# Kernel optimization log

Measured on AMD Instinct MI355X. Metric: run time of the kernel, lower is better.

Reference implementation:

```python
import jax, jax.numpy as jnp
import numpy as np

B, T, Rn, D, O, E, H, C, TM = 20, 20, 20, 4096, 16, 512, 8, 68, 1900


def l2norm(x, axis=-1, eps=1e-12):
    return x / jnp.maximum(jnp.linalg.norm(x, axis=axis, keepdims=True), eps)


def setup_inputs() -> dict:
    key = jax.random.key(0)
    ks = jax.random.split(key, 10)
    return {
        "features": jax.random.normal(ks[0], (B, T, Rn, D), jnp.float32),
        "labels": jax.random.randint(ks[1], (B, O), 0, C),
        "temporal_mem": jax.random.normal(ks[2], (TM, T, D), jnp.float32),
        "entity_W": jax.random.normal(ks[3], (C, E), jnp.float32) / np.float32(np.sqrt(C)),
        "entity_b": jnp.zeros((E,), jnp.float32),
        "Wq": jax.random.normal(ks[4], (E, E), jnp.float32) / np.float32(np.sqrt(E)),
        "Wk": jax.random.normal(ks[5], (D, E), jnp.float32) / np.float32(np.sqrt(D)),
        "Wv": jax.random.normal(ks[6], (D, E), jnp.float32) / np.float32(np.sqrt(D)),
        "Wo": jax.random.normal(ks[7], (E, E), jnp.float32) / np.float32(np.sqrt(E)),
        "obj_W1": jax.random.normal(ks[8], (D, E), jnp.float32) / np.float32(np.sqrt(D)),
        "obj_b1": jnp.zeros((E,), jnp.float32),
        "obj_W2": jax.random.normal(ks[9], (E, 1), jnp.float32) / np.float32(np.sqrt(E)),
        "obj_b2": jnp.zeros((1,), jnp.float32),
    }


def reference(features, labels, temporal_mem, entity_W, entity_b, Wq, Wk, Wv, Wo,
              obj_W1, obj_b1, obj_W2, obj_b2):
    beta = 0.5   # loss mixing weight (module's beta)
    qgce = 0.7   # generalized-CE exponent
    Dh = E // H
    # region features, L2-normalized (dataset_feat == 'CVPR' path)
    Rf = l2norm(features)                                   # [B,T,Rn,D]

    # ---- temporal memory-bank kNN retrieval ----
    R_max = l2norm(jnp.max(Rf, axis=2))                     # [B,T,D] max-pool over regions
    mem_max = l2norm(jnp.max(temporal_mem, axis=1))         # [TM,D] max-pool over frames
    sim = jnp.einsum('btd,md->btm', R_max, mem_max)         # [B,T,TM]
    idx = jnp.argmax(sim, axis=-1)                          # [B,T] nearest memory slot
    Rp = temporal_mem[idx]                                  # [B,T,T,D] gathered memory videos
    mem_feat = jnp.max(Rp, axis=2)                          # [B,T,D]

    # ---- entity (object-label) embedding: one-hot with class 0 zeroed ----
    onehot = jax.nn.one_hot(labels, C, dtype=features.dtype)
    onehot = onehot * (labels != 0)[..., None].astype(features.dtype)
    Qe = onehot @ entity_W + entity_b                       # [B,O,E]

    # ---- multi-head attention fusion over regions + retrieved memory ----
    kv = jnp.concatenate([Rf.reshape(B, T * Rn, D), mem_feat], axis=1)  # [B,N,D]
    q = (Qe @ Wq).reshape(B, O, H, Dh)
    k = (kv @ Wk).reshape(B, -1, H, Dh)
    v = (kv @ Wv).reshape(B, -1, H, Dh)
    scores = jnp.einsum('bohd,bnhd->bhon', q, k) / np.float32(np.sqrt(Dh))
    attn = jax.nn.softmax(scores, axis=-1)
    fused = jnp.einsum('bhon,bnhd->bohd', attn, v).reshape(B, O, E) @ Wo  # [B,O,E]

    # ---- top-k region objectness selection + generalized CE ----
    QR = jax.lax.stop_gradient(jnp.mean(scores, axis=1)[:, :, :T * Rn].reshape(B, O, T, Rn))
    hi = jnp.argmax(QR, axis=-1)                            # [B,O,T] top-1 region
    lo = jnp.argmin(QR, axis=-1)                            # [B,O,T] low region
    bidx = jnp.arange(B)[:, None, None]
    tidx = jnp.arange(T)[None, None, :]
    R_high = Rf[bidx, tidx, hi]                             # [B,O,T,D]
    R_low = Rf[bidx, tidx, lo]                              # [B,O,T,D]
    osel = (labels != 0).astype(features.dtype)             # [B,O]
    onum = jnp.maximum(jnp.sum(osel, axis=1), 1.0)
    mlp = lambda x: jax.nn.sigmoid(jnp.tanh(x @ obj_W1 + obj_b1) @ obj_W2 + obj_b2)
    s_hi = mlp(R_high * osel[..., None, None]).squeeze(-1)  # [B,O,T]
    s_lo = mlp(R_low * osel[..., None, None]).squeeze(-1)
    gce_hi = jnp.mean((1.0 - (s_hi + 1e-7) ** qgce) / qgce * osel[..., None], axis=-1)
    gce_lo = jnp.mean((1.0 - (1.0 - s_lo + 1e-7) ** qgce) / qgce * osel[..., None], axis=-1)
    gce = jnp.mean(jnp.sum(gce_hi, axis=1) / onum) + jnp.mean(jnp.sum(gce_lo, axis=1) / onum)

    return fused + beta * gce
```

## Files before the change

### kernel.cpp

```cpp
#include <hip/hip_runtime.h>

#define B_   20
#define T_   20
#define RN   20
#define D_   4096
#define O_   16
#define E_   512
#define H_   8
#define DH   64
#define TM_  1900
#define NKV  420
#define MROWS (B_*NKV)
#define MPAD 8448
#define NW   1536
#define NSIM 1920
#define MSIM 512
#define CAP  256
#define SIMK 4

using f32x4  = __attribute__((ext_vector_type(4))) float;
using bf16x8 = __attribute__((ext_vector_type(8))) __bf16;

__device__ __forceinline__ unsigned short f2bf(float f){
  unsigned u = __float_as_uint(f);
  u += 0x7fffu + ((u >> 16) & 1u);
  return (unsigned short)(u >> 16);
}

__device__ __forceinline__ void st_bf4(unsigned short* dst, float4 v){
  ushort4 o = make_ushort4(f2bf(v.x), f2bf(v.y), f2bf(v.z), f2bf(v.w));
  *(ushort4*)dst = o;
}

__device__ __forceinline__ float bsum256(float v, float* sh){
  int t = threadIdx.x;
  for (int o = 32; o; o >>= 1) v += __shfl_down(v, o, 64);
  __syncthreads();
  if ((t & 63) == 0) sh[t >> 6] = v;
  __syncthreads();
  return sh[0] + sh[1] + sh[2] + sh[3];
}

__device__ __forceinline__ float bmax256(float v, float* sh){
  int t = threadIdx.x;
  for (int o = 32; o; o >>= 1) v = fmaxf(v, __shfl_down(v, o, 64));
  __syncthreads();
  if ((t & 63) == 0) sh[t >> 6] = v;
  __syncthreads();
  return fmaxf(fmaxf(sh[0], sh[1]), fmaxf(sh[2], sh[3]));
}

__device__ __forceinline__ void gld16(const void* g, void* l){
  __builtin_amdgcn_global_load_lds(
      (const __attribute__((address_space(1))) unsigned int*)g,
      (__attribute__((address_space(3))) unsigned int*)l, 16, 0, 0);
}

__global__ __launch_bounds__(256) void k_wt(const float* __restrict__ Wk, const float* __restrict__ Wv,
                                            const float* __restrict__ W1, unsigned short* __restrict__ Wall){
  __shared__ float tile[32][33];
  int kb = blockIdx.x * 32, nb = blockIdx.y * 32;
  const float* src; int nc0;
  if (nb < 512)      { src = Wk; nc0 = nb; }
  else if (nb < 1024){ src = Wv; nc0 = nb - 512; }
  else               { src = W1; nc0 = nb - 1024; }
  int tx = threadIdx.x, ty = threadIdx.y;
  for (int j = 0; j < 4; ++j){
    int k = kb + ty + j*8;
    tile[ty + j*8][tx] = src[(size_t)k*E_ + nc0 + tx];
  }
  __syncthreads();
  for (int j = 0; j < 4; ++j){
    int n = nb + ty + j*8;
    int k = kb + tx;
    Wall[(size_t)n*D_ + k] = f2bf(tile[tx][ty + j*8]);
  }
}

__global__ __launch_bounds__(256) void k_region(const float* __restrict__ F, unsigned short* __restrict__ A,
                                                float* __restrict__ rmaxr, float* __restrict__ rmsum,
                                                unsigned short* __restrict__ ubf){
  int bt = blockIdx.x, t = threadIdx.x;
  if (bt >= 400){
    int4 z = make_int4(0,0,0,0);
    int4* row = (int4*)(ubf + (size_t)bt*D_);
    row[t] = z; row[t + 256] = z;
    return;
  }
  int b = bt / T_, tt = bt % T_;
  const float* fb = F + (size_t)bt*RN*D_;
  unsigned short* ab = A + ((size_t)b*NKV + (size_t)tt*RN)*D_;
  __shared__ float sh[4];
  float4 mx[4];
#pragma unroll
  for (int i = 0; i < 4; ++i) mx[i] = make_float4(-1e30f,-1e30f,-1e30f,-1e30f);
  for (int r = 0; r < RN; ++r){
    float4 v[4];
    float s = 0.f;
#pragma unroll
    for (int i = 0; i < 4; ++i){
      v[i] = *(const float4*)(fb + (size_t)r*D_ + i*1024 + t*4);
      s += v[i].x*v[i].x + v[i].y*v[i].y + v[i].z*v[i].z + v[i].w*v[i].w;
    }
    s = bsum256(s, sh);
    float ri = 1.f / fmaxf(sqrtf(s), 1e-12f);
#pragma unroll
    for (int i = 0; i < 4; ++i){
      v[i].x *= ri; v[i].y *= ri; v[i].z *= ri; v[i].w *= ri;
      st_bf4(ab + (size_t)r*D_ + i*1024 + t*4, v[i]);
      mx[i].x = fmaxf(mx[i].x, v[i].x); mx[i].y = fmaxf(mx[i].y, v[i].y);
      mx[i].z = fmaxf(mx[i].z, v[i].z); mx[i].w = fmaxf(mx[i].w, v[i].w);
    }
  }
  float s2 = 0.f;
#pragma unroll
  for (int i = 0; i < 4; ++i){
    *(float4*)(rmaxr + (size_t)bt*D_ + i*1024 + t*4) = mx[i];
    s2 += mx[i].x*mx[i].x + mx[i].y*mx[i].y + mx[i].z*mx[i].z + mx[i].w*mx[i].w;
  }
  s2 = bsum256(s2, sh);
  if (t == 0) rmsum[bt] = s2;
  float inv = 1.f / fmaxf(sqrtf(s2), 1e-12f);
#pragma unroll
  for (int i = 0; i < 4; ++i){
    float4 u = mx[i];
    u.x *= inv; u.y *= inv; u.z *= inv; u.w *= inv;
    st_bf4(ubf + (size_t)bt*D_ + i*1024 + t*4, u);
  }
}

__global__ __launch_bounds__(256) void k_mempool(const float* __restrict__ TMm, float* __restrict__ umax,
                                                 float* __restrict__ msum, unsigned short* __restrict__ wnorm){
  int m = blockIdx.x, t = threadIdx.x;
  if (m >= TM_){
    int4 z = make_int4(0,0,0,0);
    int4* row = (int4*)(wnorm + (size_t)m*D_);
    row[t] = z; row[t + 256] = z;
    return;
  }
  const float* base = TMm + (size_t)m*T_*D_;
  float4 mx[4];
#pragma unroll
  for (int i = 0; i < 4; ++i) mx[i] = make_float4(-1e30f,-1e30f,-1e30f,-1e30f);
  for (int f = 0; f < T_; ++f){
#pragma unroll
    for (int i = 0; i < 4; ++i){
      float4 v = *(const float4*)(base + (size_t)f*D_ + i*1024 + t*4);
      mx[i].x = fmaxf(mx[i].x, v.x); mx[i].y = fmaxf(mx[i].y, v.y);
      mx[i].z = fmaxf(mx[i].z, v.z); mx[i].w = fmaxf(mx[i].w, v.w);
    }
  }
  float s = 0.f;
#pragma unroll
  for (int i = 0; i < 4; ++i){
    *(float4*)(umax + (size_t)m*D_ + i*1024 + t*4) = mx[i];
    s += mx[i].x*mx[i].x + mx[i].y*mx[i].y + mx[i].z*mx[i].z + mx[i].w*mx[i].w;
  }
  __shared__ float sh[4];
  s = bsum256(s, sh);
  if (t == 0) msum[m] = s;
  float inv = 1.f / fmaxf(sqrtf(s), 1e-12f);
#pragma unroll
  for (int i = 0; i < 4; ++i){
    float4 u = mx[i];
    u.x *= inv; u.y *= inv; u.z *= inv; u.w *= inv;
    st_bf4(wnorm + (size_t)m*D_ + i*1024 + t*4, u);
  }
}

__global__ __launch_bounds__(256, 2) void k_gemm(const unsigned short* __restrict__ A,
                                                 const unsigned short* __restrict__ Bw,
                                                 float* __restrict__ C,
                                                 int nNt, int ldc, int doswz, int nwg,
                                                 int nblk, int nkt, size_t cpart){
  __shared__ char lds[32768];
  int part = blockIdx.x / nblk;
  int bid  = blockIdx.x % nblk;
  if (doswz){ int q = nwg >> 3; bid = (bid & 7)*q + (bid >> 3); }
  int mt = bid / nNt, nt = bid % nNt;
  int tid = threadIdx.x, wv = tid >> 6, l = tid & 63;
  int wr = (wv >> 1) * 64, wc = (wv & 1) * 64;
  const char* Ab = (const char*)A + (size_t)mt*128*(size_t)(D_*2);
  const char* Bb = (const char*)Bw + (size_t)nt*128*(size_t)(D_*2);
  C += (size_t)part * cpart;
  f32x4 acc[4][4];
#pragma unroll
  for (int m = 0; m < 4; ++m)
#pragma unroll
    for (int n = 0; n < 4; ++n) acc[m][n] = (f32x4){0.f,0.f,0.f,0.f};
  int kt0 = part * nkt;
  for (int kt = kt0; kt < kt0 + nkt; ++kt){
    int ktoff = kt*128;
#pragma unroll
    for (int i = 0; i < 4; ++i){
      int idx = i*256 + tid;
      int row = idx >> 3, u = idx & 7;
      int ul = u ^ (row & 7);
      gld16(Ab + (size_t)row*(D_*2) + ktoff + ul*16, lds + i*4096 + wv*1024);
      gld16(Bb + (size_t)row*(D_*2) + ktoff + ul*16, lds + 16384 + i*4096 + wv*1024);
    }
    __syncthreads();
#pragma unroll
    for (int kk = 0; kk < 2; ++kk){
      bf16x8 av[4], bv[4];
#pragma unroll
      for (int m = 0; m < 4; ++m){
        int row = wr + m*16 + (l & 15);
        int u = (kk*4 + (l >> 4)) ^ (row & 7);
        av[m] = *(const bf16x8*)(lds + row*128 + u*16);
      }
#pragma unroll
      for (int n = 0; n < 4; ++n){
        int row = wc + n*16 + (l & 15);
        int u = (kk*4 + (l >> 4)) ^ (row & 7);
        bv[n] = *(const bf16x8*)(lds + 16384 + row*128 + u*16);
      }
#pragma unroll
      for (int m = 0; m < 4; ++m)
#pragma unroll
        for (int n = 0; n < 4; ++n)
          acc[m][n] = __builtin_amdgcn_mfma_f32_16x16x32_bf16(av[m], bv[n], acc[m][n], 0, 0, 0);
    }
    __syncthreads();
  }
  int rq = (l >> 4) * 4, cq = l & 15;
  size_t crow0 = (size_t)mt*128 + wr, ccol0 = (size_t)nt*128 + wc;
#pragma unroll
  for (int m = 0; m < 4; ++m)
#pragma unroll
    for (int n = 0; n < 4; ++n){
      size_t r0 = crow0 + m*16 + rq, c0 = ccol0 + n*16 + cq;
#pragma unroll
      for (int j = 0; j < 4; ++j)
        C[(r0 + j)*ldc + c0] = acc[m][n][j];
    }
}

__global__ __launch_bounds__(256) void k_pick(const float* __restrict__ simp,
                                              const float* __restrict__ rmaxr, const float* __restrict__ rmsum,
                                              const float* __restrict__ umax, const float* __restrict__ msum,
                                              unsigned short* __restrict__ A){
  int bt = blockIdx.x, t = threadIdx.x;
  if (bt >= 400){
    int4 z = make_int4(0,0,0,0);
    int4* row = (int4*)(A + (size_t)(MROWS + bt - 400)*D_);
    row[t] = z; row[t + 256] = z;
    return;
  }
  __shared__ float srow[NSIM];
  __shared__ float sh[4];
  __shared__ int cnt;
  __shared__ int cl[CAP];
  for (int m = t; m < NSIM; m += 256){
    float s = 0.f;
#pragma unroll
    for (int p = 0; p < SIMK; ++p)
      s += simp[(size_t)p*MSIM*NSIM + (size_t)bt*NSIM + m];
    srow[m] = s;
  }
  if (t == 0) cnt = 0;
  __syncthreads();
  float mx = -1e30f;
  for (int m = t; m < TM_; m += 256) mx = fmaxf(mx, srow[m]);
  mx = bmax256(mx, sh);
  float thr = mx - 2.5e-4f;
  for (int m = t; m < TM_; m += 256){
    if (srow[m] >= thr){
      int p = atomicAdd(&cnt, 1);
      if (p < CAP) cl[p] = m;
    }
  }
  __syncthreads();
  int cn = cnt < CAP ? cnt : CAP;
  float rinvv = 1.f / fmaxf(sqrtf(rmsum[bt]), 1e-12f);
  const float* a = rmaxr + (size_t)bt*D_;
  float best = -1e30f; int bestm = 0;
  for (int ci = 0; ci < cn; ++ci){
    int m = cl[ci];
    const float* wrow = umax + (size_t)m*D_;
    float p = 0.f;
    for (int i = t*4; i < D_; i += 1024){
      float4 av = *(const float4*)(a + i);
      float4 wv = *(const float4*)(wrow + i);
      p += av.x*wv.x + av.y*wv.y + av.z*wv.z + av.w*wv.w;
    }
    p = bsum256(p, sh);
    float sim = p * rinvv * (1.f / fmaxf(sqrtf(msum[m]), 1e-12f));
    if (sim > best || (sim == best && m < bestm) || ci == 0){ 
      if (sim > best || ci == 0 || (sim == best && m < bestm)){ best = sim; bestm = m; }
    }
  }
  int b = bt / T_, tt = bt % T_;
  unsigned short* dst = A + ((size_t)b*NKV + 400 + tt)*D_;
  const float* src = umax + (size_t)bestm*D_;
#pragma unroll
  for (int i = 0; i < 4; ++i){
    size_t off = (size_t)i*1024 + t*4;
    float4 v = *(const float4*)(src + off);
    st_bf4(dst + off, v);
  }
}

__global__ __launch_bounds__(256) void k_q(const int* __restrict__ labels, const float* __restrict__ entW,
                                           const float* __restrict__ entB, const float* __restrict__ Wq,
                                           float* __restrict__ q){
  int bo = blockIdx.x, t = threadIdx.x;
  __shared__ float qe[E_];
  int lab = labels[bo];
  float sel = (lab != 0) ? 1.f : 0.f;
  qe[t]       = sel * entW[(size_t)lab*E_ + t]       + entB[t];
  qe[t + 256] = sel * entW[(size_t)lab*E_ + t + 256] + entB[t + 256];
  __syncthreads();
  float a0 = 0.f, a1 = 0.f;
  for (int ep = 0; ep < E_; ++ep){
    float r = qe[ep];
    a0 += r * Wq[(size_t)ep*E_ + t];
    a1 += r * Wq[(size_t)ep*E_ + t + 256];
  }
  q[(size_t)bo*E_ + t] = a0;
  q[(size_t)bo*E_ + t + 256] = a1;
}

__global__ __launch_bounds__(256) void k_attn(const float* __restrict__ q, const float* __restrict__ c2,
                                              float* __restrict__ fpre){
  int bh = blockIdx.x; int b = bh >> 3, h = bh & 7;
  int t = threadIdx.x, w = t >> 6, l = t & 63;
  __shared__ float qhp[O_][DH + 1];
  __shared__ float kb[105][DH + 1];
  __shared__ float sc[O_][NKV];
  for (int i = t; i < O_*DH; i += 256){
    int o = i >> 6, d = i & 63;
    qhp[o][d] = q[((size_t)(b*O_ + o))*E_ + h*DH + d] * 0.125f;
  }
  __syncthreads();
  for (int c = 0; c < 4; ++c){
    for (int i = t; i < 105*DH; i += 256){
      int j = i >> 6, d = i & 63;
      kb[j][d] = c2[((size_t)(b*NKV + c*105 + j))*NW + h*DH + d];
    }
    __syncthreads();
    for (int i = t; i < O_*105; i += 256){
      int o = i / 105, j = i % 105;
      float acc = 0.f;
      for (int d = 0; d < DH; ++d) acc += qhp[o][d] * kb[j][d];
      sc[o][c*105 + j] = acc;
    }
    __syncthreads();
  }
  for (int oi = 0; oi < 4; ++oi){
    int o = w + oi*4;
    float mx = -1e30f;
    for (int n = l; n < NKV; n += 64) mx = fmaxf(mx, sc[o][n]);
    for (int off = 32; off; off >>= 1) mx = fmaxf(mx, __shfl_xor(mx, off, 64));
    float sum = 0.f;
    for (int n = l; n < NKV; n += 64){ float e = expf(sc[o][n] - mx); sc[o][n] = e; sum += e; }
    for (int off = 32; off; off >>= 1) sum += __shfl_xor(sum, off, 64);
    float inv = 1.f / sum;
    for (int n = l; n < NKV; n += 64) sc[o][n] *= inv;
  }
  __syncthreads();
  float acc[4] = {0.f, 0.f, 0.f, 0.f};
  for (int c = 0; c < 4; ++c){
    for (int i = t; i < 105*DH; i += 256){
      int j = i >> 6, d = i & 63;
      kb[j][d] = c2[((size_t)(b*NKV + c*105 + j))*NW + E_ + h*DH + d];
    }
    __syncthreads();
#pragma unroll
    for (int og = 0; og < 4; ++og){
      int o = og*4 + w;
      float a = 0.f;
      for (int j = 0; j < 105; ++j) a += sc[o][c*105 + j] * kb[j][l];
      acc[og] += a;
    }
    __syncthreads();
  }
#pragma unroll
  for (int og = 0; og < 4; ++og){
    int o = og*4 + w;
    fpre[((size_t)(b*O_ + o))*E_ + h*DH + l] = acc[og];
  }
}

__global__ __launch_bounds__(256) void k_hilo(const float* __restrict__ q, const float* __restrict__ c2,
                                              int* __restrict__ hi, int* __restrict__ lo){
  int bid = blockIdx.x;
  int b = bid / T_, tt = bid % T_;
  int t = threadIdx.x;
  __shared__ float kl[RN][E_ + 1];
  __shared__ float qr[O_][RN];
  for (int i = t; i < RN*E_; i += 256){
    int r = i >> 9, e = i & 511;
    kl[r][e] = c2[((size_t)(b*NKV + tt*RN + r))*NW + e];
  }
  __syncthreads();
#pragma unroll
  for (int pp = 0; pp < 2; ++pp){
    int p = t + pp*256;
    if (p < O_*RN){
      int o = p / RN, r = p % RN;
      const float* qrow = q + ((size_t)(b*O_ + o))*E_;
      float acc = 0.f;
      for (int e = 0; e < E_; ++e) acc += qrow[e] * kl[r][e];
      qr[o][r] = acc;
    }
  }
  __syncthreads();
  if (t < O_){
    int o = t;
    float bh = qr[o][0], bl = qr[o][0]; int ih = 0, il = 0;
#pragma unroll
    for (int r = 1; r < RN; ++r){
      float v = qr[o][r];
      if (v > bh){ bh = v; ih = r; }
      if (v < bl){ bl = v; il = r; }
    }
    int rowbase = b*NKV + tt*RN;
    int outi = (b*O_ + o)*T_ + tt;
    hi[outi] = rowbase + ih;
    lo[outi] = rowbase + il;
  }
}

__global__ __launch_bounds__(256) void k_z(const float* __restrict__ c2, const float* __restrict__ b1,
                                           const float* __restrict__ W2, const float* __restrict__ b2,
                                           float* __restrict__ z){
  int g = blockIdx.x*4 + (threadIdx.x >> 6);
  int l = threadIdx.x & 63;
  int b = g / 400, j = g % 400;
  int row = b*NKV + j;
  const float* hrow = c2 + (size_t)row*NW + 1024;
  float acc = 0.f;
  for (int e = l; e < E_; e += 64) acc += tanhf(hrow[e] + b1[e]) * W2[e];
  for (int off = 32; off; off >>= 1) acc += __shfl_down(acc, off, 64);
  if (l == 0) z[row] = 1.f / (1.f + expf(-(acc + b2[0])));
}

__global__ __launch_bounds__(256) void k_gce(const float* __restrict__ z, const int* __restrict__ hi,
                                             const int* __restrict__ lo, const int* __restrict__ labels,
                                             float* __restrict__ gout){
  __shared__ float vb[B_];
  __shared__ int cb[B_];
  int t = threadIdx.x;
  if (t < B_){ vb[t] = 0.f; cb[t] = 0; }
  __syncthreads();
  for (int p = t; p < B_*O_; p += 256){
    int b = p / O_;
    if (labels[p] != 0){
      float acc = 0.f;
      for (int tt = 0; tt < T_; ++tt){
        float shi = z[hi[p*T_ + tt]];
        float slo = z[lo[p*T_ + tt]];
        acc += (1.f - __powf(shi + 1e-7f, 0.7f)) / 0.7f;
        acc += (1.f - __powf(1.f - slo + 1e-7f, 0.7f)) / 0.7f;
      }
      atomicAdd(&vb[b], acc / (float)T_);
      atomicAdd(&cb[b], 1);
    }
  }
  __syncthreads();
  if (t == 0){
    float g = 0.f;
    for (int b = 0; b < B_; ++b) g += vb[b] / fmaxf((float)cb[b], 1.f);
    gout[0] = 0.5f * (g / (float)B_);
  }
}

__global__ __launch_bounds__(256) void k_out(const float* __restrict__ fpre, const float* __restrict__ Wo,
                                             const float* __restrict__ gce, float* __restrict__ out){
  int bo = blockIdx.x, t = threadIdx.x;
  __shared__ float row[E_];
  row[t] = fpre[(size_t)bo*E_ + t];
  row[t + 256] = fpre[(size_t)bo*E_ + t + 256];
  __syncthreads();
  float g = gce[0];
  float a0 = 0.f, a1 = 0.f;
  for (int ep = 0; ep < E_; ++ep){
    float r = row[ep];
    a0 += r * Wo[(size_t)ep*E_ + t];
    a1 += r * Wo[(size_t)ep*E_ + t + 256];
  }
  out[(size_t)bo*E_ + t] = a0 + g;
  out[(size_t)bo*E_ + t + 256] = a1 + g;
}

extern "C" void kernel_launch(void* const* d_in, const int* in_sizes, int n_in,
                              void* d_out, int out_size, void* d_ws, size_t ws_size,
                              hipStream_t stream) {
  (void)in_sizes; (void)n_in; (void)out_size; (void)ws_size;
  const float* F    = (const float*)d_in[0];
  const int*   labels = (const int*)d_in[1];
  const float* TMm  = (const float*)d_in[2];
  const float* entW = (const float*)d_in[3];
  const float* entB = (const float*)d_in[4];
  const float* Wq   = (const float*)d_in[5];
  const float* Wk   = (const float*)d_in[6];
  const float* Wv   = (const float*)d_in[7];
  const float* Wo   = (const float*)d_in[8];
  const float* W1   = (const float*)d_in[9];
  const float* b1   = (const float*)d_in[10];
  const float* W2   = (const float*)d_in[11];
  const float* b2   = (const float*)d_in[12];
  float* out = (float*)d_out;

  size_t off = 0;
  char* wsb = (char*)d_ws;
  auto alloc = [&](size_t bytes) -> char* {
    char* p = wsb + off; off += (bytes + 255) & ~(size_t)255; return p;
  };
  unsigned short* A_kv = (unsigned short*)alloc((size_t)MPAD * D_ * 2);
  unsigned short* Wall = (unsigned short*)alloc((size_t)NW * D_ * 2);
  float* umax          = (float*)alloc((size_t)TM_ * D_ * 4);
  char*  c2reg         = alloc((size_t)MPAD * NW * 4);
  float* C2    = (float*)c2reg;
  unsigned short* wnorm = (unsigned short*)c2reg;
  float* simp  = (float*)(c2reg + 15728640);
  unsigned short* ubf = (unsigned short*)(c2reg + 31457280);
  float* rmaxr = (float*)(c2reg + 35651584);
  float* qbuf  = (float*)alloc((size_t)B_ * O_ * E_ * 4);
  float* fpre  = (float*)alloc((size_t)B_ * O_ * E_ * 4);
  float* rmsum = (float*)alloc(400 * 4);
  float* msum  = (float*)alloc(TM_ * 4);
  int*   hib   = (int*)alloc(6400 * 4);
  int*   lob   = (int*)alloc(6400 * 4);
  float* zbuf  = (float*)alloc((size_t)MROWS * 4);
  float* gbuf  = (float*)alloc(256);

  k_wt<<<dim3(D_/32, NW/32), dim3(32, 8), 0, stream>>>(Wk, Wv, W1, Wall);
  k_region<<<MSIM, 256, 0, stream>>>(F, A_kv, rmaxr, rmsum, ubf);
  k_mempool<<<NSIM/128*128 == NSIM ? NSIM : NSIM, 256, 0, stream>>>(TMm, umax, msum, wnorm);
  k_gemm<<<(MSIM/128)*(NSIM/128)*SIMK, 256, 0, stream>>>(ubf, wnorm, simp, NSIM/128, NSIM, 0, 60,
                                                         (MSIM/128)*(NSIM/128), (D_/64)/SIMK,
                                                         (size_t)MSIM*NSIM);
  k_pick<<<448, 256, 0, stream>>>(simp, rmaxr, rmsum, umax, msum, A_kv);
  k_gemm<<<(MPAD/128)*(NW/128), 256, 0, stream>>>(A_kv, Wall, C2, NW/128, NW, 1,
                                                  (MPAD/128)*(NW/128),
                                                  (MPAD/128)*(NW/128), D_/64, 0);
  k_q<<<B_*O_, 256, 0, stream>>>(labels, entW, entB, Wq, qbuf);
  k_attn<<<B_*H_, 256, 0, stream>>>(qbuf, C2, fpre);
  k_hilo<<<B_*T_, 256, 0, stream>>>(qbuf, C2, hib, lob);
  k_z<<<2000, 256, 0, stream>>>(C2, b1, W2, b2, zbuf);
  k_gce<<<1, 256, 0, stream>>>(zbuf, hib, lob, labels, gbuf);
  k_out<<<B_*O_, 256, 0, stream>>>(fpre, Wo, gbuf, out);
}
```

Measured before the change: 577.0 us.

## Merge independent kernels into multi-role launches and raise sim-GEMM split-K

Folds k_wt, k_region, k_mempool and k_q into one k_pre launch, with block ranges selecting each role. Folds k_attn, k_hilo and k_z into one k_post launch, and merges the GCE reduction into the output projection kernel. This cuts launch count and lets independent work overlap. Split-K for the similarity GEMM goes from 4 to 8, and ubf/rmaxr get their own workspace buffers so they no longer alias the C2 region. Risks: k_post reserves the largest shared-memory footprint for every block, which can lower occupancy for its light roles. Also, each k_outg block redundantly recomputes the GCE reduction.

```diff
diff --git a/kernel.cpp b/kernel.cpp
--- a/kernel.cpp
+++ b/kernel.cpp
@@ -16,7 +16,7 @@
 #define NSIM 1920
 #define MSIM 512
 #define CAP  256
-#define SIMK 4
+#define SIMK 8
 
 using f32x4  = __attribute__((ext_vector_type(4))) float;
 using bf16x8 = __attribute__((ext_vector_type(8))) __bf16;
@@ -56,115 +56,138 @@
       (__attribute__((address_space(3))) unsigned int*)l, 16, 0, 0);
 }
 
-__global__ __launch_bounds__(256) void k_wt(const float* __restrict__ Wk, const float* __restrict__ Wv,
-                                            const float* __restrict__ W1, unsigned short* __restrict__ Wall){
-  __shared__ float tile[32][33];
-  int kb = blockIdx.x * 32, nb = blockIdx.y * 32;
-  const float* src; int nc0;
-  if (nb < 512)      { src = Wk; nc0 = nb; }
-  else if (nb < 1024){ src = Wv; nc0 = nb - 512; }
-  else               { src = W1; nc0 = nb - 1024; }
-  int tx = threadIdx.x, ty = threadIdx.y;
-  for (int j = 0; j < 4; ++j){
-    int k = kb + ty + j*8;
-    tile[ty + j*8][tx] = src[(size_t)k*E_ + nc0 + tx];
-  }
-  __syncthreads();
-  for (int j = 0; j < 4; ++j){
-    int n = nb + ty + j*8;
-    int k = kb + tx;
-    Wall[(size_t)n*D_ + k] = f2bf(tile[tx][ty + j*8]);
-  }
-}
-
-__global__ __launch_bounds__(256) void k_region(const float* __restrict__ F, unsigned short* __restrict__ A,
-                                                float* __restrict__ rmaxr, float* __restrict__ rmsum,
-                                                unsigned short* __restrict__ ubf){
-  int bt = blockIdx.x, t = threadIdx.x;
-  if (bt >= 400){
-    int4 z = make_int4(0,0,0,0);
-    int4* row = (int4*)(ubf + (size_t)bt*D_);
-    row[t] = z; row[t + 256] = z;
-    return;
-  }
-  int b = bt / T_, tt = bt % T_;
-  const float* fb = F + (size_t)bt*RN*D_;
-  unsigned short* ab = A + ((size_t)b*NKV + (size_t)tt*RN)*D_;
-  __shared__ float sh[4];
-  float4 mx[4];
-#pragma unroll
-  for (int i = 0; i < 4; ++i) mx[i] = make_float4(-1e30f,-1e30f,-1e30f,-1e30f);
-  for (int r = 0; r < RN; ++r){
-    float4 v[4];
+__global__ __launch_bounds__(256) void k_pre(
+    const float* __restrict__ F, const float* __restrict__ TMm,
+    const float* __restrict__ Wk, const float* __restrict__ Wv, const float* __restrict__ W1,
+    unsigned short* __restrict__ Wall,
+    unsigned short* __restrict__ A, float* __restrict__ rmaxr, float* __restrict__ rmsum,
+    unsigned short* __restrict__ ubf,
+    float* __restrict__ umax, float* __restrict__ msum, unsigned short* __restrict__ wnorm,
+    const int* __restrict__ labels, const float* __restrict__ entW, const float* __restrict__ entB,
+    const float* __restrict__ Wq, float* __restrict__ q){
+  __shared__ char smem[4352];
+  int bid = blockIdx.x, t = threadIdx.x;
+  if (bid < 1920){
+    int m = bid;
+    if (m >= TM_){
+      int4 zz = make_int4(0,0,0,0);
+      int4* row = (int4*)(wnorm + (size_t)m*D_);
+      row[t] = zz; row[t + 256] = zz;
+      return;
+    }
+    float* sh = (float*)smem;
+    const float* base = TMm + (size_t)m*T_*D_;
+    float4 mx[4];
+#pragma unroll
+    for (int i = 0; i < 4; ++i) mx[i] = make_float4(-1e30f,-1e30f,-1e30f,-1e30f);
+    for (int f = 0; f < T_; ++f){
+#pragma unroll
+      for (int i = 0; i < 4; ++i){
+        float4 v = *(const float4*)(base + (size_t)f*D_ + i*1024 + t*4);
+        mx[i].x = fmaxf(mx[i].x, v.x); mx[i].y = fmaxf(mx[i].y, v.y);
+        mx[i].z = fmaxf(mx[i].z, v.z); mx[i].w = fmaxf(mx[i].w, v.w);
+      }
+    }
     float s = 0.f;
 #pragma unroll
     for (int i = 0; i < 4; ++i){
-      v[i] = *(const float4*)(fb + (size_t)r*D_ + i*1024 + t*4);
-      s += v[i].x*v[i].x + v[i].y*v[i].y + v[i].z*v[i].z + v[i].w*v[i].w;
+      *(float4*)(umax + (size_t)m*D_ + i*1024 + t*4) = mx[i];
+      s += mx[i].x*mx[i].x + mx[i].y*mx[i].y + mx[i].z*mx[i].z + mx[i].w*mx[i].w;
     }
     s = bsum256(s, sh);
-    float ri = 1.f / fmaxf(sqrtf(s), 1e-12f);
+    if (t == 0) msum[m] = s;
+    float inv = 1.f / fmaxf(sqrtf(s), 1e-12f);
 #pragma unroll
     for (int i = 0; i < 4; ++i){
-      v[i].x *= ri; v[i].y *= ri; v[i].z *= ri; v[i].w *= ri;
-      st_bf4(ab + (size_t)r*D_ + i*1024 + t*4, v[i]);
-      mx[i].x = fmaxf(mx[i].x, v[i].x); mx[i].y = fmaxf(mx[i].y, v[i].y);
-      mx[i].z = fmaxf(mx[i].z, v[i].z); mx[i].w = fmaxf(mx[i].w, v[i].w);
-    }
-  }
-  float s2 = 0.f;
-#pragma unroll
-  for (int i = 0; i < 4; ++i){
-    *(float4*)(rmaxr + (size_t)bt*D_ + i*1024 + t*4) = mx[i];
-    s2 += mx[i].x*mx[i].x + mx[i].y*mx[i].y + mx[i].z*mx[i].z + mx[i].w*mx[i].w;
-  }
-  s2 = bsum256(s2, sh);
-  if (t == 0) rmsum[bt] = s2;
-  float inv = 1.f / fmaxf(sqrtf(s2), 1e-12f);
-#pragma unroll
-  for (int i = 0; i < 4; ++i){
-    float4 u = mx[i];
-    u.x *= inv; u.y *= inv; u.z *= inv; u.w *= inv;
-    st_bf4(ubf + (size_t)bt*D_ + i*1024 + t*4, u);
-  }
-}
-
-__global__ __launch_bounds__(256) void k_mempool(const float* __restrict__ TMm, float* __restrict__ umax,
-                                                 float* __restrict__ msum, unsigned short* __restrict__ wnorm){
-  int m = blockIdx.x, t = threadIdx.x;
-  if (m >= TM_){
-    int4 z = make_int4(0,0,0,0);
-    int4* row = (int4*)(wnorm + (size_t)m*D_);
-    row[t] = z; row[t + 256] = z;
-    return;
-  }
-  const float* base = TMm + (size_t)m*T_*D_;
-  float4 mx[4];
-#pragma unroll
-  for (int i = 0; i < 4; ++i) mx[i] = make_float4(-1e30f,-1e30f,-1e30f,-1e30f);
-  for (int f = 0; f < T_; ++f){
+      float4 u = mx[i];
+      u.x *= inv; u.y *= inv; u.z *= inv; u.w *= inv;
+      st_bf4(wnorm + (size_t)m*D_ + i*1024 + t*4, u);
+    }
+  } else if (bid < 2432){
+    int bt = bid - 1920;
+    if (bt >= 400){
+      int4 zz = make_int4(0,0,0,0);
+      int4* row = (int4*)(ubf + (size_t)bt*D_);
+      row[t] = zz; row[t + 256] = zz;
+      return;
+    }
+    float* sh = (float*)smem;
+    int b = bt / T_, tt = bt % T_;
+    const float* fb = F + (size_t)bt*RN*D_;
+    unsigned short* ab = A + ((size_t)b*NKV + (size_t)tt*RN)*D_;
+    float4 mx[4];
+#pragma unroll
+    for (int i = 0; i < 4; ++i) mx[i] = make_float4(-1e30f,-1e30f,-1e30f,-1e30f);
+    for (int r = 0; r < RN; ++r){
+      float4 v[4];
+      float s = 0.f;
+#pragma unroll
+      for (int i = 0; i < 4; ++i){
+        v[i] = *(const float4*)(fb + (size_t)r*D_ + i*1024 + t*4);
+        s += v[i].x*v[i].x + v[i].y*v[i].y + v[i].z*v[i].z + v[i].w*v[i].w;
+      }
+      s = bsum256(s, sh);
+      float ri = 1.f / fmaxf(sqrtf(s), 1e-12f);
+#pragma unroll
+      for (int i = 0; i < 4; ++i){
+        v[i].x *= ri; v[i].y *= ri; v[i].z *= ri; v[i].w *= ri;
+        st_bf4(ab + (size_t)r*D_ + i*1024 + t*4, v[i]);
+        mx[i].x = fmaxf(mx[i].x, v[i].x); mx[i].y = fmaxf(mx[i].y, v[i].y);
+        mx[i].z = fmaxf(mx[i].z, v[i].z); mx[i].w = fmaxf(mx[i].w, v[i].w);
+      }
+    }
+    float s2 = 0.f;
 #pragma unroll
     for (int i = 0; i < 4; ++i){
-      float4 v = *(const float4*)(base + (size_t)f*D_ + i*1024 + t*4);
-      mx[i].x = fmaxf(mx[i].x, v.x); mx[i].y = fmaxf(mx[i].y, v.y);
-      mx[i].z = fmaxf(mx[i].z, v.z); mx[i].w = fmaxf(mx[i].w, v.w);
-    }
-  }
-  float s = 0.f;
-#pragma unroll
-  for (int i = 0; i < 4; ++i){
-    *(float4*)(umax + (size_t)m*D_ + i*1024 + t*4) = mx[i];
-    s += mx[i].x*mx[i].x + mx[i].y*mx[i].y + mx[i].z*mx[i].z + mx[i].w*mx[i].w;
-  }
-  __shared__ float sh[4];
-  s = bsum256(s, sh);
-  if (t == 0) msum[m] = s;
-  float inv = 1.f / fmaxf(sqrtf(s), 1e-12f);
-#pragma unroll
-  for (int i = 0; i < 4; ++i){
-    float4 u = mx[i];
-    u.x *= inv; u.y *= inv; u.z *= inv; u.w *= inv;
-    st_bf4(wnorm + (size_t)m*D_ + i*1024 + t*4, u);
+      *(float4*)(rmaxr + (size_t)bt*D_ + i*1024 + t*4) = mx[i];
+      s2 += mx[i].x*mx[i].x + mx[i].y*mx[i].y + mx[i].z*mx[i].z + mx[i].w*mx[i].w;
+    }
+    s2 = bsum256(s2, sh);
+    if (t == 0) rmsum[bt] = s2;
+    float inv = 1.f / fmaxf(sqrtf(s2), 1e-12f);
+#pragma unroll
+    for (int i = 0; i < 4; ++i){
+      float4 u = mx[i];
+      u.x *= inv; u.y *= inv; u.z *= inv; u.w *= inv;
+      st_bf4(ubf + (size_t)bt*D_ + i*1024 + t*4, u);
+    }
+  } else if (bid < 8576){
+    int wti = bid - 2432;
+    float* tile = (float*)smem;
+    int kb = (wti & 127) * 32, nb = (wti >> 7) * 32;
+    const float* src; int nc0;
+    if (nb < 512)      { src = Wk; nc0 = nb; }
+    else if (nb < 1024){ src = Wv; nc0 = nb - 512; }
+    else               { src = W1; nc0 = nb - 1024; }
+    int tx = t & 31, ty = t >> 5;
+#pragma unroll
+    for (int j = 0; j < 4; ++j){
+      int k = kb + ty + j*8;
+      tile[(ty + j*8)*33 + tx] = src[(size_t)k*E_ + nc0 + tx];
+    }
+    __syncthreads();
+#pragma unroll
+    for (int j = 0; j < 4; ++j){
+      int n = nb + ty + j*8;
+      int k = kb + tx;
+      Wall[(size_t)n*D_ + k] = f2bf(tile[tx*33 + ty + j*8]);
+    }
+  } else {
+    int bo = bid - 8576;
+    float* qe = (float*)smem;
+    int lab = labels[bo];
+    float sel = (lab != 0) ? 1.f : 0.f;
+    qe[t]       = sel * entW[(size_t)lab*E_ + t]       + entB[t];
+    qe[t + 256] = sel * entW[(size_t)lab*E_ + t + 256] + entB[t + 256];
+    __syncthreads();
+    float a0 = 0.f, a1 = 0.f;
+    for (int ep = 0; ep < E_; ++ep){
+      float r = qe[ep];
+      a0 += r * Wq[(size_t)ep*E_ + t];
+      a1 += r * Wq[(size_t)ep*E_ + t + 256];
+    }
+    q[(size_t)bo*E_ + t] = a0;
+    q[(size_t)bo*E_ + t + 256] = a1;
   }
 }
 
@@ -274,7 +297,7 @@
   int cn = cnt < CAP ? cnt : CAP;
   float rinvv = 1.f / fmaxf(sqrtf(rmsum[bt]), 1e-12f);
   const float* a = rmaxr + (size_t)bt*D_;
-  float best = -1e30f; int bestm = 0;
+  float best = -1e30f; int bestm = 0x7fffffff;
   for (int ci = 0; ci < cn; ++ci){
     int m = cl[ci];
     const float* wrow = umax + (size_t)m*D_;
@@ -286,9 +309,7 @@
     }
     p = bsum256(p, sh);
     float sim = p * rinvv * (1.f / fmaxf(sqrtf(msum[m]), 1e-12f));
-    if (sim > best || (sim == best && m < bestm) || ci == 0){ 
-      if (sim > best || ci == 0 || (sim == best && m < bestm)){ best = sim; bestm = m; }
-    }
+    if (sim > best || (sim == best && m < bestm)){ best = sim; bestm = m; }
   }
   int b = bt / T_, tt = bt % T_;
   unsigned short* dst = A + ((size_t)b*NKV + 400 + tt)*D_;
@@ -301,147 +322,131 @@
   }
 }
 
-__global__ __launch_bounds__(256) void k_q(const int* __restrict__ labels, const float* __restrict__ entW,
-                                           const float* __restrict__ entB, const float* __restrict__ Wq,
-                                           float* __restrict__ q){
-  int bo = blockIdx.x, t = threadIdx.x;
-  __shared__ float qe[E_];
-  int lab = labels[bo];
-  float sel = (lab != 0) ? 1.f : 0.f;
-  qe[t]       = sel * entW[(size_t)lab*E_ + t]       + entB[t];
-  qe[t + 256] = sel * entW[(size_t)lab*E_ + t + 256] + entB[t + 256];
-  __syncthreads();
-  float a0 = 0.f, a1 = 0.f;
-  for (int ep = 0; ep < E_; ++ep){
-    float r = qe[ep];
-    a0 += r * Wq[(size_t)ep*E_ + t];
-    a1 += r * Wq[(size_t)ep*E_ + t + 256];
-  }
-  q[(size_t)bo*E_ + t] = a0;
-  q[(size_t)bo*E_ + t + 256] = a1;
-}
-
-__global__ __launch_bounds__(256) void k_attn(const float* __restrict__ q, const float* __restrict__ c2,
-                                              float* __restrict__ fpre){
-  int bh = blockIdx.x; int b = bh >> 3, h = bh & 7;
-  int t = threadIdx.x, w = t >> 6, l = t & 63;
-  __shared__ float qhp[O_][DH + 1];
-  __shared__ float kb[105][DH + 1];
-  __shared__ float sc[O_][NKV];
-  for (int i = t; i < O_*DH; i += 256){
-    int o = i >> 6, d = i & 63;
-    qhp[o][d] = q[((size_t)(b*O_ + o))*E_ + h*DH + d] * 0.125f;
-  }
-  __syncthreads();
-  for (int c = 0; c < 4; ++c){
-    for (int i = t; i < 105*DH; i += 256){
-      int j = i >> 6, d = i & 63;
-      kb[j][d] = c2[((size_t)(b*NKV + c*105 + j))*NW + h*DH + d];
-    }
-    __syncthreads();
-    for (int i = t; i < O_*105; i += 256){
-      int o = i / 105, j = i % 105;
-      float acc = 0.f;
-      for (int d = 0; d < DH; ++d) acc += qhp[o][d] * kb[j][d];
-      sc[o][c*105 + j] = acc;
-    }
-    __syncthreads();
-  }
-  for (int oi = 0; oi < 4; ++oi){
-    int o = w + oi*4;
-    float mx = -1e30f;
-    for (int n = l; n < NKV; n += 64) mx = fmaxf(mx, sc[o][n]);
-    for (int off = 32; off; off >>= 1) mx = fmaxf(mx, __shfl_xor(mx, off, 64));
-    float sum = 0.f;
-    for (int n = l; n < NKV; n += 64){ float e = expf(sc[o][n] - mx); sc[o][n] = e; sum += e; }
-    for (int off = 32; off; off >>= 1) sum += __shfl_xor(sum, off, 64);
-    float inv = 1.f / sum;
-    for (int n = l; n < NKV; n += 64) sc[o][n] *= inv;
-  }
-  __syncthreads();
-  float acc[4] = {0.f, 0.f, 0.f, 0.f};
-  for (int c = 0; c < 4; ++c){
-    for (int i = t; i < 105*DH; i += 256){
-      int j = i >> 6, d = i & 63;
-      kb[j][d] = c2[((size_t)(b*NKV + c*105 + j))*NW + E_ + h*DH + d];
-    }
-    __syncthreads();
+__global__ __launch_bounds__(256) void k_post(const float* __restrict__ q, const float* __restrict__ c2,
+                                              float* __restrict__ fpre, int* __restrict__ hi,
+                                              int* __restrict__ lo, const float* __restrict__ b1,
+                                              const float* __restrict__ W2, const float* __restrict__ b2,
+                                              float* __restrict__ z){
+  __shared__ char smem[58368];
+  int bid = blockIdx.x, t = threadIdx.x;
+  if (bid < 160){
+    int b = bid >> 3, h = bid & 7;
+    int w = t >> 6, l = t & 63;
+    float* qhp = (float*)smem;
+    float* kb  = (float*)(smem + 4160);
+    float* sc  = (float*)(smem + 31460);
+    for (int i = t; i < O_*DH; i += 256){
+      int o = i >> 6, d = i & 63;
+      qhp[o*65 + d] = q[((size_t)(b*O_ + o))*E_ + h*DH + d] * 0.125f;
+    }
+    __syncthreads();
+    for (int c = 0; c < 4; ++c){
+      for (int i = t; i < 105*DH; i += 256){
+        int j = i >> 6, d = i & 63;
+        kb[j*65 + d] = c2[((size_t)(b*NKV + c*105 + j))*NW + h*DH + d];
+      }
+      __syncthreads();
+      for (int i = t; i < O_*105; i += 256){
+        int o = i / 105, j = i % 105;
+        float acc = 0.f;
+        for (int d = 0; d < DH; ++d) acc += qhp[o*65 + d] * kb[j*65 + d];
+        sc[o*420 + c*105 + j] = acc;
+      }
+      __syncthreads();
+    }
+    for (int oi = 0; oi < 4; ++oi){
+      int o = w + oi*4;
+      float mx = -1e30f;
+      for (int n = l; n < NKV; n += 64) mx = fmaxf(mx, sc[o*420 + n]);
+      for (int of = 32; of; of >>= 1) mx = fmaxf(mx, __shfl_xor(mx, of, 64));
+      float sum = 0.f;
+      for (int n = l; n < NKV; n += 64){ float e = expf(sc[o*420 + n] - mx); sc[o*420 + n] = e; sum += e; }
+      for (int of = 32; of; of >>= 1) sum += __shfl_xor(sum, of, 64);
+      float inv = 1.f / sum;
+      for (int n = l; n < NKV; n += 64) sc[o*420 + n] *= inv;
+    }
+    __syncthreads();
+    float acc[4] = {0.f, 0.f, 0.f, 0.f};
+    for (int c = 0; c < 4; ++c){
+      for (int i = t; i < 105*DH; i += 256){
+        int j = i >> 6, d = i & 63;
+        kb[j*65 + d] = c2[((size_t)(b*NKV + c*105 + j))*NW + E_ + h*DH + d];
+      }
+      __syncthreads();
+#pragma unroll
+      for (int og = 0; og < 4; ++og){
+        int o = og*4 + w;
+        float a = 0.f;
+        for (int j = 0; j < 105; ++j) a += sc[o*420 + c*105 + j] * kb[j*65 + l];
+        acc[og] += a;
+      }
+      __syncthreads();
+    }
 #pragma unroll
     for (int og = 0; og < 4; ++og){
       int o = og*4 + w;
-      float a = 0.f;
-      for (int j = 0; j < 105; ++j) a += sc[o][c*105 + j] * kb[j][l];
-      acc[og] += a;
-    }
-    __syncthreads();
-  }
-#pragma unroll
-  for (int og = 0; og < 4; ++og){
-    int o = og*4 + w;
-    fpre[((size_t)(b*O_ + o))*E_ + h*DH + l] = acc[og];
-  }
-}
-
-__global__ __launch_bounds__(256) void k_hilo(const float* __restrict__ q, const float* __restrict__ c2,
-                                              int* __restrict__ hi, int* __restrict__ lo){
-  int bid = blockIdx.x;
-  int b = bid / T_, tt = bid % T_;
-  int t = threadIdx.x;
-  __shared__ float kl[RN][E_ + 1];
-  __shared__ float qr[O_][RN];
-  for (int i = t; i < RN*E_; i += 256){
-    int r = i >> 9, e = i & 511;
-    kl[r][e] = c2[((size_t)(b*NKV + tt*RN + r))*NW + e];
-  }
-  __syncthreads();
-#pragma unroll
-  for (int pp = 0; pp < 2; ++pp){
-    int p = t + pp*256;
-    if (p < O_*RN){
-      int o = p / RN, r = p % RN;
-      const float* qrow = q + ((size_t)(b*O_ + o))*E_;
-      float acc = 0.f;
-      for (int e = 0; e < E_; ++e) acc += qrow[e] * kl[r][e];
-      qr[o][r] = acc;
-    }
-  }
-  __syncthreads();
-  if (t < O_){
-    int o = t;
-    float bh = qr[o][0], bl = qr[o][0]; int ih = 0, il = 0;
-#pragma unroll
-    for (int r = 1; r < RN; ++r){
-      float v = qr[o][r];
-      if (v > bh){ bh = v; ih = r; }
-      if (v < bl){ bl = v; il = r; }
-    }
-    int rowbase = b*NKV + tt*RN;
-    int outi = (b*O_ + o)*T_ + tt;
-    hi[outi] = rowbase + ih;
-    lo[outi] = rowbase + il;
-  }
-}
-
-__global__ __launch_bounds__(256) void k_z(const float* __restrict__ c2, const float* __restrict__ b1,
-                                           const float* __restrict__ W2, const float* __restrict__ b2,
-                                           float* __restrict__ z){
-  int g = blockIdx.x*4 + (threadIdx.x >> 6);
-  int l = threadIdx.x & 63;
-  int b = g / 400, j = g % 400;
-  int row = b*NKV + j;
-  const float* hrow = c2 + (size_t)row*NW + 1024;
-  float acc = 0.f;
-  for (int e = l; e < E_; e += 64) acc += tanhf(hrow[e] + b1[e]) * W2[e];
-  for (int off = 32; off; off >>= 1) acc += __shfl_down(acc, off, 64);
-  if (l == 0) z[row] = 1.f / (1.f + expf(-(acc + b2[0])));
-}
-
-__global__ __launch_bounds__(256) void k_gce(const float* __restrict__ z, const int* __restrict__ hi,
-                                             const int* __restrict__ lo, const int* __restrict__ labels,
-                                             float* __restrict__ gout){
+      fpre[((size_t)(b*O_ + o))*E_ + h*DH + l] = acc[og];
+    }
+  } else if (bid < 560){
+    int bt = bid - 160;
+    int b = bt / T_, tt = bt % T_;
+    float* kl = (float*)smem;
+    float* qr = (float*)(smem + 41040);
+    for (int i = t; i < RN*E_; i += 256){
+      int r = i >> 9, e = i & 511;
+      kl[r*513 + e] = c2[((size_t)(b*NKV + tt*RN + r))*NW + e];
+    }
+    __syncthreads();
+#pragma unroll
+    for (int pp = 0; pp < 2; ++pp){
+      int p = t + pp*256;
+      if (p < O_*RN){
+        int o = p / RN, r = p % RN;
+        const float* qrow = q + ((size_t)(b*O_ + o))*E_;
+        float acc = 0.f;
+        for (int e = 0; e < E_; ++e) acc += qrow[e] * kl[r*513 + e];
+        qr[o*20 + r] = acc;
+      }
+    }
+    __syncthreads();
+    if (t < O_){
+      int o = t;
+      float bh = qr[o*20], bl = qr[o*20]; int ih = 0, il = 0;
+#pragma unroll
+      for (int r = 1; r < RN; ++r){
+        float v = qr[o*20 + r];
+        if (v > bh){ bh = v; ih = r; }
+        if (v < bl){ bl = v; il = r; }
+      }
+      int rowbase = b*NKV + tt*RN;
+      int outi = (b*O_ + o)*T_ + tt;
+      hi[outi] = rowbase + ih;
+      lo[outi] = rowbase + il;
+    }
+  } else {
+    int g = (bid - 560)*4 + (t >> 6);
+    int l = t & 63;
+    int b = g / 400, j = g % 400;
+    int row = b*NKV + j;
+    const float* hrow = c2 + (size_t)row*NW + 1024;
+    float acc = 0.f;
+    for (int e = l; e < E_; e += 64) acc += tanhf(hrow[e] + b1[e]) * W2[e];
+    for (int of = 32; of; of >>= 1) acc += __shfl_down(acc, of, 64);
+    if (l == 0) z[row] = 1.f / (1.f + expf(-(acc + b2[0])));
+  }
+}
+
+__global__ __launch_bounds__(256) void k_outg(const float* __restrict__ fpre, const float* __restrict__ Wo,
+                                              const float* __restrict__ z, const int* __restrict__ hi,
+                                              const int* __restrict__ lo, const int* __restrict__ labels,
+                                              float* __restrict__ out){
+  int bo = blockIdx.x, t = threadIdx.x;
+  __shared__ float rowv[E_];
   __shared__ float vb[B_];
   __shared__ int cb[B_];
-  int t = threadIdx.x;
+  __shared__ float gsh;
+  rowv[t] = fpre[(size_t)bo*E_ + t];
+  rowv[t + 256] = fpre[(size_t)bo*E_ + t + 256];
   if (t < B_){ vb[t] = 0.f; cb[t] = 0; }
   __syncthreads();
   for (int p = t; p < B_*O_; p += 256){
@@ -462,21 +467,13 @@
   if (t == 0){
     float g = 0.f;
     for (int b = 0; b < B_; ++b) g += vb[b] / fmaxf((float)cb[b], 1.f);
-    gout[0] = 0.5f * (g / (float)B_);
-  }
-}
-
-__global__ __launch_bounds__(256) void k_out(const float* __restrict__ fpre, const float* __restrict__ Wo,
-                                             const float* __restrict__ gce, float* __restrict__ out){
-  int bo = blockIdx.x, t = threadIdx.x;
-  __shared__ float row[E_];
-  row[t] = fpre[(size_t)bo*E_ + t];
-  row[t + 256] = fpre[(size_t)bo*E_ + t + 256];
-  __syncthreads();
-  float g = gce[0];
+    gsh = 0.5f * (g / (float)B_);
+  }
+  __syncthreads();
+  float g = gsh;
   float a0 = 0.f, a1 = 0.f;
   for (int ep = 0; ep < E_; ++ep){
-    float r = row[ep];
+    float r = rowv[ep];
     a0 += r * Wo[(size_t)ep*E_ + t];
     a1 += r * Wo[(size_t)ep*E_ + t + 256];
   }
@@ -515,8 +512,8 @@
   float* C2    = (float*)c2reg;
   unsigned short* wnorm = (unsigned short*)c2reg;
   float* simp  = (float*)(c2reg + 15728640);
-  unsigned short* ubf = (unsigned short*)(c2reg + 31457280);
-  float* rmaxr = (float*)(c2reg + 35651584);
+  unsigned short* ubf = (unsigned short*)alloc((size_t)MSIM * D_ * 2);
+  float* rmaxr = (float*)alloc((size_t)400 * D_ * 4);
   float* qbuf  = (float*)alloc((size_t)B_ * O_ * E_ * 4);
   float* fpre  = (float*)alloc((size_t)B_ * O_ * E_ * 4);
   float* rmsum = (float*)alloc(400 * 4);
@@ -524,11 +521,9 @@
   int*   hib   = (int*)alloc(6400 * 4);
   int*   lob   = (int*)alloc(6400 * 4);
   float* zbuf  = (float*)alloc((size_t)MROWS * 4);
-  float* gbuf  = (float*)alloc(256);
-
-  k_wt<<<dim3(D_/32, NW/32), dim3(32, 8), 0, stream>>>(Wk, Wv, W1, Wall);
-  k_region<<<MSIM, 256, 0, stream>>>(F, A_kv, rmaxr, rmsum, ubf);
-  k_mempool<<<NSIM/128*128 == NSIM ? NSIM : NSIM, 256, 0, stream>>>(TMm, umax, msum, wnorm);
+
+  k_pre<<<8896, 256, 0, stream>>>(F, TMm, Wk, Wv, W1, Wall, A_kv, rmaxr, rmsum, ubf,
+                                  umax, msum, wnorm, labels, entW, entB, Wq, qbuf);
   k_gemm<<<(MSIM/128)*(NSIM/128)*SIMK, 256, 0, stream>>>(ubf, wnorm, simp, NSIM/128, NSIM, 0, 60,
                                                          (MSIM/128)*(NSIM/128), (D_/64)/SIMK,
                                                          (size_t)MSIM*NSIM);
@@ -536,10 +531,6 @@
   k_gemm<<<(MPAD/128)*(NW/128), 256, 0, stream>>>(A_kv, Wall, C2, NW/128, NW, 1,
                                                   (MPAD/128)*(NW/128),
                                                   (MPAD/128)*(NW/128), D_/64, 0);
-  k_q<<<B_*O_, 256, 0, stream>>>(labels, entW, entB, Wq, qbuf);
-  k_attn<<<B_*H_, 256, 0, stream>>>(qbuf, C2, fpre);
-  k_hilo<<<B_*T_, 256, 0, stream>>>(qbuf, C2, hib, lob);
-  k_z<<<2000, 256, 0, stream>>>(C2, b1, W2, b2, zbuf);
-  k_gce<<<1, 256, 0, stream>>>(zbuf, hib, lob, labels, gbuf);
-  k_out<<<B_*O_, 256, 0, stream>>>(fpre, Wo, gbuf, out);
-}
+  k_post<<<2560, 256, 0, stream>>>(qbuf, C2, fpre, hib, lob, b1, W2, b2, zbuf);
+  k_outg<<<B_*O_, 256, 0, stream>>>(fpre, Wo, zbuf, hib, lob, labels, out);
+}
```

Measured after the change: 510.7 us. 1.13x faster.
